# Optimization experiments

Hardware: AMD Instinct MI355X
Metric: run time of the kernel (lower is better)

The kernel has to match this reference:

```python
import jax, jax.numpy as jnp
import numpy as np

N = 20000   # nodes
E = 320000  # edges (before self-loops)
F_IN = 128  # in_feats
H = 4       # heads
C = 64      # hidden (per-head channels; concat=False averages heads)
G = 64      # graphs in batch
EPS = 1e-5  # BatchNorm eps


def _gat(x, src, dst, W, a_src, a_dst, bias):
    # PyG GATConv, concat=False: project, per-edge LeakyReLU attention,
    # segment-softmax over destination nodes, scatter-add, mean over heads.
    h = (x @ W).reshape(N, H, C)                    # [N,H,C]
    es = (h * a_src).sum(-1)                        # [N,H]
    ed = (h * a_dst).sum(-1)                        # [N,H]
    e = jax.nn.leaky_relu(es[src] + ed[dst], 0.2)   # [Etot,H]
    m = jax.ops.segment_max(e, dst, num_segments=N)
    m = jnp.where(jnp.isfinite(m), m, 0.0)          # nodes with no in-edges
    p = jnp.exp(e - m[dst])
    s = jax.ops.segment_sum(p, dst, num_segments=N)
    alpha = p / (s[dst] + 1e-16)                    # PyG softmax epsilon
    out = jax.ops.segment_sum(h[src] * alpha[:, :, None], dst, num_segments=N)
    return out.mean(axis=1) + bias                  # [N,C]


def _bn(x, g, b):
    # BatchNorm1d in training mode: biased batch statistics over nodes
    mu = x.mean(axis=0)
    var = ((x - mu) ** 2).mean(axis=0)
    return (x - mu) * jax.lax.rsqrt(var + EPS) * g + b


def setup_inputs() -> dict:
    key = jax.random.key(0)
    ks = jax.random.split(key, 16)
    x = jax.random.normal(ks[0], (N, F_IN), dtype=jnp.float32)
    edge_index = jax.random.randint(ks[1], (2, E), 0, N, dtype=jnp.int32)
    batch_idx = jnp.sort(jax.random.randint(ks[2], (N,), 0, G, dtype=jnp.int32))
    s1 = 1.0 / np.sqrt(F_IN)
    s2 = 1.0 / np.sqrt(C)
    return {
        "x": x,
        "W1": jax.random.normal(ks[3], (F_IN, H * C), jnp.float32) * s1,
        "a_src1": jax.random.normal(ks[4], (H, C), jnp.float32) * s2,
        "a_dst1": jax.random.normal(ks[5], (H, C), jnp.float32) * s2,
        "b1": jnp.zeros((C,), jnp.float32),
        "Wskip": jax.random.normal(ks[6], (F_IN, C), jnp.float32) * s1,
        "bskip": jnp.zeros((C,), jnp.float32),
        "g1": jnp.ones((C,), jnp.float32),
        "be1": jnp.zeros((C,), jnp.float32),
        "W2": jax.random.normal(ks[7], (C, H * C), jnp.float32) * s2,
        "a_src2": jax.random.normal(ks[8], (H, C), jnp.float32) * s2,
        "a_dst2": jax.random.normal(ks[9], (H, C), jnp.float32) * s2,
        "b2": jnp.zeros((C,), jnp.float32),
        "g2": jnp.ones((C,), jnp.float32),
        "be2": jnp.zeros((C,), jnp.float32),
        "edge_index": edge_index,
        "batch_idx": batch_idx,
    }


def reference(x, W1, a_src1, a_dst1, b1, Wskip, bskip, g1, be1,
              W2, a_src2, a_dst2, b2, g2, be2, edge_index, batch_idx):
    # add self-loops (PyG GATConv default add_self_loops=True)
    loop = jnp.arange(N, dtype=edge_index.dtype)
    src = jnp.concatenate([edge_index[0], loop])
    dst = jnp.concatenate([edge_index[1], loop])

    x0 = x
    h = _gat(x, src, dst, W1, a_src1, a_dst1, b1)
    h = jax.nn.gelu(_bn(h, g1, be1) + x0 @ Wskip + bskip, approximate=False)
    # dropout is identity in eval mode
    h2 = _gat(h, src, dst, W2, a_src2, a_dst2, b2)
    h2 = jax.nn.gelu(_bn(h2, g2, be2) + h, approximate=False)

    # global mean pool over graphs
    sums = jax.ops.segment_sum(h2, batch_idx, num_segments=G)
    cnts = jax.ops.segment_sum(jnp.ones((N,), h2.dtype), batch_idx, num_segments=G)
    return sums / jnp.maximum(cnts, 1.0)[:, None]
```

## Files before the change

### kernel.cpp

```cpp
#include <hip/hip_runtime.h>
#include <math.h>

#define NN   20000
#define EE   320000
#define ETOT 340000
#define FIN  128
#define HH   4
#define CC   64
#define HC   256
#define GG   64
#define BN_EPS 1e-5f
#define S1   384
#define S2   320
#define NBUCK 64
#define MAXDEG 64

typedef _Float16 v8h __attribute__((ext_vector_type(8)));
typedef _Float16 v4h __attribute__((ext_vector_type(4)));
typedef float    v4f __attribute__((ext_vector_type(4)));

__device__ __forceinline__ unsigned short f2bf(float f) {
    unsigned u = __float_as_uint(f);
    unsigned r = (u + 0x7FFF + ((u >> 16) & 1)) >> 16;
    return (unsigned short)r;
}
__device__ __forceinline__ float bf2f(unsigned short u) {
    return __uint_as_float((unsigned)u << 16);
}
__device__ __forceinline__ float gelu_exact(float v) {
    return 0.5f * v * (1.f + erff(v * 0.70710678118654752f));
}

__global__ __launch_bounds__(256) void pre1_kernel(
        const int* __restrict__ bidx, int* __restrict__ gstart,
        const float* __restrict__ W1, const float* __restrict__ Wskip,
        const float* __restrict__ W2,
        const float* __restrict__ as1, const float* __restrict__ ad1,
        const float* __restrict__ as2, const float* __restrict__ ad2,
        _Float16* __restrict__ BT1, _Float16* __restrict__ BT2,
        int* __restrict__ deg, float* __restrict__ sbuck1,
        float* __restrict__ sbuck2, float* __restrict__ outz) {
    int b = blockIdx.x, t = threadIdx.x;
    if (b < 79) {
        int i = b * 256 + t;
        if (i >= NN) return;
        int cur = bidx[i];
        if (i == 0) { for (int g = 0; g <= cur; ++g) gstart[g] = 0; }
        else { int prev = bidx[i - 1]; for (int g = prev + 1; g <= cur; ++g) gstart[g] = i; }
        if (i == NN - 1) { for (int g = cur + 1; g <= GG; ++g) gstart[g] = NN; }
    } else if (b < 271) {
        int i = (b - 79) * 256 + t;
        int col = i >> 7, k = i & 127;
        float v;
        if (col < 256) {
            v = W1[k * 256 + col];
        } else if (col < 320) {
            v = Wskip[k * 64 + (col - 256)];
        } else if (col < 328) {
            int kk = col - 320, h = kk & 3;
            const float* av = (kk < 4 ? as1 : ad1) + h * 64;
            const float* wr = W1 + k * 256 + h * 64;
            float s = 0.f;
            #pragma unroll 8
            for (int c = 0; c < 64; ++c) s += wr[c] * av[c];
            v = s;
        } else v = 0.f;
        BT1[i] = (_Float16)v;
    } else if (b < 351) {
        int i = (b - 271) * 256 + t;
        int col = i >> 6, k = i & 63;
        float v;
        if (col < 256) {
            v = W2[k * 256 + col];
        } else if (col < 264) {
            int kk = col - 256, h = kk & 3;
            const float* av = (kk < 4 ? as2 : ad2) + h * 64;
            const float* wr = W2 + k * 256 + h * 64;
            float s = 0.f;
            #pragma unroll 8
            for (int c = 0; c < 64; ++c) s += wr[c] * av[c];
            v = s;
        } else v = 0.f;
        BT2[i] = (_Float16)v;
    } else if (b < 367) {
        int i = (b - 351) * 256 + t;
        outz[i] = 0.f;
    } else if (b < 446) {
        int i = (b - 367) * 256 + t;
        if (i < NN) deg[i] = 0;
    } else if (b < 478) {
        int i = (b - 446) * 256 + t;
        sbuck1[i] = 0.f;
    } else {
        int i = (b - 478) * 256 + t;
        sbuck2[i] = 0.f;
    }
}

template<int NCB>
__global__ __launch_bounds__(256) void gemm_mfma(const float* __restrict__ A,
        const _Float16* __restrict__ BT, int M, int K,
        unsigned short* __restrict__ h4b, float* __restrict__ skipO,
        float* __restrict__ esf, float* __restrict__ edf,
        int escol0, int ngemm, int do_fill,
        const int* __restrict__ ei, int* __restrict__ deg,
        int* __restrict__ csr) {
    int b = blockIdx.x;
    int t = threadIdx.x;
    if (do_fill && b >= ngemm) {
        int i = (b - ngemm) * 256 + t;
        if (i >= ETOT) return;
        int s, d;
        if (i < EE) { s = ei[i]; d = ei[EE + i]; } else { s = i - EE; d = i - EE; }
        int p = atomicAdd(&deg[d], 1);
        if (p < MAXDEG) csr[d * MAXDEG + p] = s;
        return;
    }
    const int COLT = 2 * NCB * 16;
    __shared__ _Float16 sA[32][40];
    __shared__ _Float16 sBT[2 * NCB * 16][40];
    int row0 = b * 32;
    int wave = t >> 6, lane = t & 63;
    int l15 = lane & 15, quad = lane >> 4;
    int rb  = wave & 1;
    int cb0 = (wave >> 1) * NCB;
    v4f acc[NCB] = {};
    for (int k0 = 0; k0 < K; k0 += 32) {
        {
            int r = t >> 3, c4 = t & 7;
            int gr = row0 + r;
            float4 v0 = make_float4(0.f, 0.f, 0.f, 0.f);
            if (gr < M) v0 = *(const float4*)&A[(size_t)gr * K + k0 + c4 * 4];
            v4h hv;
            hv[0] = (_Float16)v0.x; hv[1] = (_Float16)v0.y;
            hv[2] = (_Float16)v0.z; hv[3] = (_Float16)v0.w;
            *(v4h*)&sA[r][c4 * 4] = hv;
        }
        for (int j = t; j < COLT * 4; j += 256) {
            int c = j >> 2, s = j & 3;
            *(v8h*)&sBT[c][s * 8] = *(const v8h*)&BT[(size_t)c * K + k0 + s * 8];
        }
        __syncthreads();
        v8h af = *(const v8h*)&sA[rb * 16 + l15][quad * 8];
        #pragma unroll
        for (int c = 0; c < NCB; ++c) {
            v8h bf = *(const v8h*)&sBT[(cb0 + c) * 16 + l15][quad * 8];
            acc[c] = __builtin_amdgcn_mfma_f32_16x16x32_f16(af, bf, acc[c], 0, 0, 0);
        }
        __syncthreads();
    }
    #pragma unroll
    for (int c = 0; c < NCB; ++c) {
        int gcol = (cb0 + c) * 16 + l15;
        #pragma unroll
        for (int reg = 0; reg < 4; ++reg) {
            int gr = row0 + rb * 16 + quad * 4 + reg;
            if (gr >= M) continue;
            float v = acc[c][reg];
            if (gcol < 256) {
                h4b[(size_t)gr * HC + gcol] = f2bf(v);
            } else if (skipO != nullptr && gcol < 320) {
                skipO[(size_t)gr * CC + (gcol - 256)] = v;
            } else if (gcol >= escol0 && gcol < escol0 + 8) {
                if (gcol < escol0 + 4) esf[gr * 4 + (gcol - escol0)] = v;
                else                   edf[gr * 4 + (gcol - escol0 - 4)] = v;
            }
        }
    }
}

template<int NCB>
__global__ __launch_bounds__(256) void gemm_mfma_bn(const float* __restrict__ gout,
        const float* __restrict__ skip, const float* __restrict__ sbuck,
        const float* __restrict__ g, const float* __restrict__ be,
        const float* __restrict__ bskip, float* __restrict__ hmid,
        const _Float16* __restrict__ BT, int M, int K,
        unsigned short* __restrict__ h4b,
        float* __restrict__ esf, float* __restrict__ edf, int escol0) {
    const int COLT = 2 * NCB * 16;
    __shared__ _Float16 sA[32][40];
    __shared__ _Float16 sBT[2 * NCB * 16][40];
    __shared__ float tmp[128];
    __shared__ float sscale[64], sshift[64];
    int t = threadIdx.x;
    int b = blockIdx.x;
    if (t < 128) {
        float s = 0.f;
        #pragma unroll 16
        for (int k = 0; k < NBUCK; ++k) s += sbuck[k * 128 + t];
        tmp[t] = s;
    }
    __syncthreads();
    if (t < 64) {
        float mu  = tmp[t] * (1.f / NN);
        float var = tmp[64 + t] * (1.f / NN) - mu * mu;
        float inv = rsqrtf(var + BN_EPS) * g[t];
        sscale[t] = inv;
        sshift[t] = be[t] + bskip[t] - mu * inv;
    }
    __syncthreads();
    int row0 = b * 32;
    int wave = t >> 6, lane = t & 63;
    int l15 = lane & 15, quad = lane >> 4;
    int rb  = wave & 1;
    int cb0 = (wave >> 1) * NCB;
    v4f acc[NCB] = {};
    for (int k0 = 0; k0 < K; k0 += 32) {
        {
            int r = t >> 3, c4 = t & 7;
            int gr = row0 + r;
            int cb = k0 + c4 * 4;
            float vv[4];
            if (gr < M) {
                float4 q = *(const float4*)&gout[(size_t)gr * CC + cb];
                float4 p = *(const float4*)&skip[(size_t)gr * CC + cb];
                float qa[4] = {q.x, q.y, q.z, q.w};
                float pa[4] = {p.x, p.y, p.z, p.w};
                #pragma unroll
                for (int u = 0; u < 4; ++u)
                    vv[u] = gelu_exact(qa[u] * sscale[cb + u] + sshift[cb + u] + pa[u]);
                *(float4*)&hmid[(size_t)gr * CC + cb] =
                    make_float4(vv[0], vv[1], vv[2], vv[3]);
            } else {
                vv[0] = vv[1] = vv[2] = vv[3] = 0.f;
            }
            v4h hv;
            hv[0] = (_Float16)vv[0]; hv[1] = (_Float16)vv[1];
            hv[2] = (_Float16)vv[2]; hv[3] = (_Float16)vv[3];
            *(v4h*)&sA[r][c4 * 4] = hv;
        }
        for (int j = t; j < COLT * 4; j += 256) {
            int c = j >> 2, s = j & 3;
            *(v8h*)&sBT[c][s * 8] = *(const v8h*)&BT[(size_t)c * K + k0 + s * 8];
        }
        __syncthreads();
        v8h af = *(const v8h*)&sA[rb * 16 + l15][quad * 8];
        #pragma unroll
        for (int c = 0; c < NCB; ++c) {
            v8h bf = *(const v8h*)&sBT[(cb0 + c) * 16 + l15][quad * 8];
            acc[c] = __builtin_amdgcn_mfma_f32_16x16x32_f16(af, bf, acc[c], 0, 0, 0);
        }
        __syncthreads();
    }
    #pragma unroll
    for (int c = 0; c < NCB; ++c) {
        int gcol = (cb0 + c) * 16 + l15;
        #pragma unroll
        for (int reg = 0; reg < 4; ++reg) {
            int gr = row0 + rb * 16 + quad * 4 + reg;
            if (gr >= M) continue;
            float v = acc[c][reg];
            if (gcol < 256) {
                h4b[(size_t)gr * HC + gcol] = f2bf(v);
            } else if (gcol >= escol0 && gcol < escol0 + 8) {
                if (gcol < escol0 + 4) esf[gr * 4 + (gcol - escol0)] = v;
                else                   edf[gr * 4 + (gcol - escol0 - 4)] = v;
            }
        }
    }
}

__global__ __launch_bounds__(256) void aggr_kernel(const unsigned short* __restrict__ h4b,
        const float* __restrict__ esf, const float* __restrict__ edf,
        const int* __restrict__ deg, const int* __restrict__ csr_src,
        const float* __restrict__ bias, float* __restrict__ out,
        float* __restrict__ sbuck) {
    int wave = threadIdx.x >> 6, lane = threadIdx.x & 63;
    int head = lane >> 4;
    int n = blockIdx.x * 4 + wave;
    float edn = edf[n * 4 + head];
    float4 acc = make_float4(0.f, 0.f, 0.f, 0.f);
    float ssum = 0.f;
    int dn = deg[n];
    dn = (dn < MAXDEG) ? dn : MAXDEG;
    int beg = n * MAXDEG, end = beg + dn;
    int j = beg;
    for (; j + 4 <= end; j += 4) {
        int4 s4 = *(const int4*)&csr_src[j];
        float E0 = esf[s4.x * 4 + head];
        float E1 = esf[s4.y * 4 + head];
        float E2 = esf[s4.z * 4 + head];
        float E3 = esf[s4.w * 4 + head];
        ushort4 v0 = *(const ushort4*)&h4b[(size_t)s4.x * HC + lane * 4];
        ushort4 v1 = *(const ushort4*)&h4b[(size_t)s4.y * HC + lane * 4];
        ushort4 v2 = *(const ushort4*)&h4b[(size_t)s4.z * HC + lane * 4];
        ushort4 v3 = *(const ushort4*)&h4b[(size_t)s4.w * HC + lane * 4];
        float e0 = E0 + edn; e0 = fmaxf(e0, 0.2f * e0); float w0 = __expf(e0);
        float e1 = E1 + edn; e1 = fmaxf(e1, 0.2f * e1); float w1 = __expf(e1);
        float e2 = E2 + edn; e2 = fmaxf(e2, 0.2f * e2); float w2 = __expf(e2);
        float e3 = E3 + edn; e3 = fmaxf(e3, 0.2f * e3); float w3 = __expf(e3);
        acc.x += w0 * bf2f(v0.x); acc.y += w0 * bf2f(v0.y);
        acc.z += w0 * bf2f(v0.z); acc.w += w0 * bf2f(v0.w); ssum += w0;
        acc.x += w1 * bf2f(v1.x); acc.y += w1 * bf2f(v1.y);
        acc.z += w1 * bf2f(v1.z); acc.w += w1 * bf2f(v1.w); ssum += w1;
        acc.x += w2 * bf2f(v2.x); acc.y += w2 * bf2f(v2.y);
        acc.z += w2 * bf2f(v2.z); acc.w += w2 * bf2f(v2.w); ssum += w2;
        acc.x += w3 * bf2f(v3.x); acc.y += w3 * bf2f(v3.y);
        acc.z += w3 * bf2f(v3.z); acc.w += w3 * bf2f(v3.w); ssum += w3;
    }
    for (; j < end; ++j) {
        int s = csr_src[j];
        float E = esf[s * 4 + head];
        ushort4 v = *(const ushort4*)&h4b[(size_t)s * HC + lane * 4];
        float e = E + edn; e = fmaxf(e, 0.2f * e); float w = __expf(e);
        acc.x += w * bf2f(v.x); acc.y += w * bf2f(v.y);
        acc.z += w * bf2f(v.z); acc.w += w * bf2f(v.w); ssum += w;
    }
    float inv = 1.f / (ssum + 1e-16f);
    float4 r;
    r.x = acc.x * inv; r.y = acc.y * inv; r.z = acc.z * inv; r.w = acc.w * inv;
    r.x += __shfl_xor(r.x, 16); r.y += __shfl_xor(r.y, 16);
    r.z += __shfl_xor(r.z, 16); r.w += __shfl_xor(r.w, 16);
    r.x += __shfl_xor(r.x, 32); r.y += __shfl_xor(r.y, 32);
    r.z += __shfl_xor(r.z, 32); r.w += __shfl_xor(r.w, 32);
    __shared__ float ls[4][64], lq[4][64];
    if (lane < 16) {
        float4 b4 = *(const float4*)&bias[lane * 4];
        float4 o;
        o.x = 0.25f * r.x + b4.x; o.y = 0.25f * r.y + b4.y;
        o.z = 0.25f * r.z + b4.z; o.w = 0.25f * r.w + b4.w;
        *(float4*)&out[n * CC + lane * 4] = o;
        *(float4*)&ls[wave][lane * 4] = o;
        float4 q;
        q.x = o.x * o.x; q.y = o.y * o.y; q.z = o.z * o.z; q.w = o.w * o.w;
        *(float4*)&lq[wave][lane * 4] = q;
    }
    __syncthreads();
    if (wave == 0) {
        float s = ls[0][lane] + ls[1][lane] + ls[2][lane] + ls[3][lane];
        float q = lq[0][lane] + lq[1][lane] + lq[2][lane] + lq[3][lane];
        int bk = (blockIdx.x & (NBUCK - 1)) * 128;
        atomicAdd(&sbuck[bk + lane], s);
        atomicAdd(&sbuck[bk + 64 + lane], q);
    }
}

__global__ __launch_bounds__(256) void bnapply2_kernel(const float* __restrict__ gout,
        const float* __restrict__ sbuck, const float* __restrict__ g,
        const float* __restrict__ be, const float* __restrict__ resid,
        const int* __restrict__ bidx, const int* __restrict__ gstart,
        float* __restrict__ out) {
    __shared__ float tmp[128];
    __shared__ float smu[64], sinv[64];
    __shared__ float ls[4][64];
    __shared__ int gi[4];
    int t = threadIdx.x;
    if (t < 128) {
        float s = 0.f;
        #pragma unroll 16
        for (int k = 0; k < NBUCK; ++k) s += sbuck[k * 128 + t];
        tmp[t] = s;
    }
    __syncthreads();
    if (t < 64) {
        float mu  = tmp[t] * (1.f / NN);
        float var = tmp[64 + t] * (1.f / NN) - mu * mu;
        smu[t] = mu;
        sinv[t] = rsqrtf(var + BN_EPS) * g[t];
    }
    __syncthreads();
    int i = blockIdx.x * 256 + t;
    int ch = i & 63;
    int wave = t >> 6;
    int n = i >> 6;
    float v = (gout[i] - smu[ch]) * sinv[ch] + be[ch] + resid[i];
    v = gelu_exact(v);
    int gg = bidx[n];
    int cnt = gstart[gg + 1] - gstart[gg];
    ls[wave][ch] = v * (1.f / (float)cnt);
    if (ch == 0) gi[wave] = gg;
    __syncthreads();
    if (wave == 0) {
        if (gi[0] == gi[1] && gi[1] == gi[2] && gi[2] == gi[3]) {
            float s = ls[0][ch] + ls[1][ch] + ls[2][ch] + ls[3][ch];
            atomicAdd(&out[gi[0] * CC + ch], s);
        } else {
            #pragma unroll
            for (int w2 = 0; w2 < 4; ++w2)
                atomicAdd(&out[gi[w2] * CC + ch], ls[w2][ch]);
        }
    }
}

extern "C" void kernel_launch(void* const* d_in, const int* in_sizes, int n_in,
                              void* d_out, int out_size, void* d_ws, size_t ws_size,
                              hipStream_t stream) {
    const float* x      = (const float*)d_in[0];
    const float* W1     = (const float*)d_in[1];
    const float* a_src1 = (const float*)d_in[2];
    const float* a_dst1 = (const float*)d_in[3];
    const float* b1     = (const float*)d_in[4];
    const float* Wskip  = (const float*)d_in[5];
    const float* bskip  = (const float*)d_in[6];
    const float* g1     = (const float*)d_in[7];
    const float* be1    = (const float*)d_in[8];
    const float* W2     = (const float*)d_in[9];
    const float* a_src2 = (const float*)d_in[10];
    const float* a_dst2 = (const float*)d_in[11];
    const float* b2     = (const float*)d_in[12];
    const float* g2     = (const float*)d_in[13];
    const float* be2    = (const float*)d_in[14];
    const int*   ei     = (const int*)d_in[15];
    const int*   bidx   = (const int*)d_in[16];
    float* out = (float*)d_out;

    char* w = (char*)d_ws;
    size_t o = 0;
    auto alloc = [&](size_t bytes) -> void* {
        void* p = w + o;
        o = (o + bytes + 255) & ~(size_t)255;
        return p;
    };

    unsigned short* h4b = (unsigned short*)alloc((size_t)NN * HC * 2);
    float* esf = (float*)alloc((size_t)NN * 16);
    float* edf = (float*)alloc((size_t)NN * 16);
    float* skip = (float*)alloc((size_t)NN * CC * 4);
    float* gout = (float*)alloc((size_t)NN * CC * 4);
    float* hmid = (float*)alloc((size_t)NN * CC * 4);
    _Float16* BT1 = (_Float16*)alloc((size_t)S1 * FIN * 2);
    _Float16* BT2 = (_Float16*)alloc((size_t)S2 * CC * 2);
    int* csr    = (int*)alloc((size_t)NN * MAXDEG * 4);
    int* gstart = (int*)alloc((size_t)(GG + 1) * 4);
    int* deg      = (int*)alloc((size_t)NN * 4);
    float* sbuck1 = (float*)alloc((size_t)NBUCK * 128 * 4);
    float* sbuck2 = (float*)alloc((size_t)NBUCK * 128 * 4);

    int ebk = (ETOT + 255) / 256;
    int ngemm = (NN + 31) / 32;
    int nodeblk = NN / 4;

    pre1_kernel<<<510, 256, 0, stream>>>(bidx, gstart,
            W1, Wskip, W2, a_src1, a_dst1, a_src2, a_dst2, BT1, BT2,
            deg, sbuck1, sbuck2, out);

    gemm_mfma<12><<<ngemm + ebk, 256, 0, stream>>>(x, BT1, NN, FIN,
            h4b, skip, esf, edf, 320, ngemm, 1, ei, deg, csr);
    aggr_kernel<<<nodeblk, 256, 0, stream>>>(h4b, esf, edf, deg, csr, b1, gout,
            sbuck1);

    gemm_mfma_bn<10><<<ngemm, 256, 0, stream>>>(gout, skip, sbuck1, g1, be1, bskip,
            hmid, BT2, NN, CC, h4b, esf, edf, 256);
    aggr_kernel<<<nodeblk, 256, 0, stream>>>(h4b, esf, edf, deg, csr, b2, gout,
            sbuck2);
    bnapply2_kernel<<<NN * CC / 256, 256, 0, stream>>>(
        gout, sbuck2, g2, be2, hmid, bidx, gstart, out);
}
```

Measured before the change: 202.6 us.

## Load full K slab once and keep B fragments in registers for MFMA GEMMs

The two projection GEMMs are restructured. Instead of looping over K in 32-wide chunks with a shared-memory B tile and two barriers per step, each block stages the whole 32-row A slab into LDS once. Each wave loads its B fragments straight from global memory into registers and computes both 16-row halves, so every B fragment is reused across two row tiles. The row bounds checks are dropped because N divides evenly by 32, and fewer barriers and LDS round trips are intended. In exchange, register pressure rises and the kernels become specialised to fixed sizes.

After: 212.5 us. 4.9% more time.

```diff
diff --git a/kernel.cpp b/kernel.cpp
--- a/kernel.cpp
+++ b/kernel.cpp
@@ -97,17 +97,15 @@
     }
 }
 
-template<int NCB>
-__global__ __launch_bounds__(256) void gemm_mfma(const float* __restrict__ A,
-        const _Float16* __restrict__ BT, int M, int K,
+__global__ __launch_bounds__(256) void gemm1_kernel(const float* __restrict__ A,
+        const _Float16* __restrict__ BT,
         unsigned short* __restrict__ h4b, float* __restrict__ skipO,
         float* __restrict__ esf, float* __restrict__ edf,
-        int escol0, int ngemm, int do_fill,
-        const int* __restrict__ ei, int* __restrict__ deg,
+        int ngemm, const int* __restrict__ ei, int* __restrict__ deg,
         int* __restrict__ csr) {
     int b = blockIdx.x;
     int t = threadIdx.x;
-    if (do_fill && b >= ngemm) {
+    if (b >= ngemm) {
         int i = (b - ngemm) * 256 + t;
         if (i >= ETOT) return;
         int s, d;
@@ -116,70 +114,78 @@
         if (p < MAXDEG) csr[d * MAXDEG + p] = s;
         return;
     }
-    const int COLT = 2 * NCB * 16;
-    __shared__ _Float16 sA[32][40];
-    __shared__ _Float16 sBT[2 * NCB * 16][40];
+    __shared__ _Float16 sA[32][136];
     int row0 = b * 32;
+    {
+        int r = t >> 3, k0 = (t & 7) * 16;
+        const float* src = &A[(size_t)(row0 + r) * FIN + k0];
+        float4 f0 = *(const float4*)&src[0];
+        float4 f1 = *(const float4*)&src[4];
+        float4 f2 = *(const float4*)&src[8];
+        float4 f3 = *(const float4*)&src[12];
+        v8h h0, h1;
+        h0[0] = (_Float16)f0.x; h0[1] = (_Float16)f0.y;
+        h0[2] = (_Float16)f0.z; h0[3] = (_Float16)f0.w;
+        h0[4] = (_Float16)f1.x; h0[5] = (_Float16)f1.y;
+        h0[6] = (_Float16)f1.z; h0[7] = (_Float16)f1.w;
+        h1[0] = (_Float16)f2.x; h1[1] = (_Float16)f2.y;
+        h1[2] = (_Float16)f2.z; h1[3] = (_Float16)f2.w;
+        h1[4] = (_Float16)f3.x; h1[5] = (_Float16)f3.y;
+        h1[6] = (_Float16)f3.z; h1[7] = (_Float16)f3.w;
+        *(v8h*)&sA[r][k0]     = h0;
+        *(v8h*)&sA[r][k0 + 8] = h1;
+    }
     int wave = t >> 6, lane = t & 63;
     int l15 = lane & 15, quad = lane >> 4;
-    int rb  = wave & 1;
-    int cb0 = (wave >> 1) * NCB;
-    v4f acc[NCB] = {};
-    for (int k0 = 0; k0 < K; k0 += 32) {
-        {
-            int r = t >> 3, c4 = t & 7;
-            int gr = row0 + r;
-            float4 v0 = make_float4(0.f, 0.f, 0.f, 0.f);
-            if (gr < M) v0 = *(const float4*)&A[(size_t)gr * K + k0 + c4 * 4];
-            v4h hv;
-            hv[0] = (_Float16)v0.x; hv[1] = (_Float16)v0.y;
-            hv[2] = (_Float16)v0.z; hv[3] = (_Float16)v0.w;
-            *(v4h*)&sA[r][c4 * 4] = hv;
+    int cb0 = wave * 6;
+    v8h bf[6][4];
+    #pragma unroll
+    for (int c = 0; c < 6; ++c)
+        #pragma unroll
+        for (int k = 0; k < 4; ++k)
+            bf[c][k] = *(const v8h*)&BT[(size_t)((cb0 + c) * 16 + l15) * FIN + k * 32 + quad * 8];
+    __syncthreads();
+    v4f acc[2][6] = {};
+    #pragma unroll
+    for (int k = 0; k < 4; ++k) {
+        v8h a0 = *(const v8h*)&sA[l15][k * 32 + quad * 8];
+        v8h a1 = *(const v8h*)&sA[16 + l15][k * 32 + quad * 8];
+        #pragma unroll
+        for (int c = 0; c < 6; ++c) {
+            acc[0][c] = __builtin_amdgcn_mfma_f32_16x16x32_f16(a0, bf[c][k], acc[0][c], 0, 0, 0);
+            acc[1][c] = __builtin_amdgcn_mfma_f32_16x16x32_f16(a1, bf[c][k], acc[1][c], 0, 0, 0);
         }
-        for (int j = t; j < COLT * 4; j += 256) {
-            int c = j >> 2, s = j & 3;
-            *(v8h*)&sBT[c][s * 8] = *(const v8h*)&BT[(size_t)c * K + k0 + s * 8];
-        }
-        __syncthreads();
-        v8h af = *(const v8h*)&sA[rb * 16 + l15][quad * 8];
-        #pragma unroll
-        for (int c = 0; c < NCB; ++c) {
-            v8h bf = *(const v8h*)&sBT[(cb0 + c) * 16 + l15][quad * 8];
-            acc[c] = __builtin_amdgcn_mfma_f32_16x16x32_f16(af, bf, acc[c], 0, 0, 0);
-        }
-        __syncthreads();
-    }
-    #pragma unroll
-    for (int c = 0; c < NCB; ++c) {
-        int gcol = (cb0 + c) * 16 + l15;
-        #pragma unroll
-        for (int reg = 0; reg < 4; ++reg) {
-            int gr = row0 + rb * 16 + quad * 4 + reg;
-            if (gr >= M) continue;
-            float v = acc[c][reg];
-            if (gcol < 256) {
-                h4b[(size_t)gr * HC + gcol] = f2bf(v);
-            } else if (skipO != nullptr && gcol < 320) {
-                skipO[(size_t)gr * CC + (gcol - 256)] = v;
-            } else if (gcol >= escol0 && gcol < escol0 + 8) {
-                if (gcol < escol0 + 4) esf[gr * 4 + (gcol - escol0)] = v;
-                else                   edf[gr * 4 + (gcol - escol0 - 4)] = v;
+    }
+    #pragma unroll
+    for (int rb = 0; rb < 2; ++rb) {
+        #pragma unroll
+        for (int c = 0; c < 6; ++c) {
+            int gcol = (cb0 + c) * 16 + l15;
+            #pragma unroll
+            for (int reg = 0; reg < 4; ++reg) {
+                int gr = row0 + rb * 16 + quad * 4 + reg;
+                float v = acc[rb][c][reg];
+                if (gcol < 256) {
+                    h4b[(size_t)gr * HC + gcol] = f2bf(v);
+                } else if (gcol < 320) {
+                    skipO[(size_t)gr * CC + (gcol - 256)] = v;
+                } else if (gcol < 328) {
+                    if (gcol < 324) esf[gr * 4 + (gcol - 320)] = v;
+                    else            edf[gr * 4 + (gcol - 324)] = v;
+                }
             }
         }
     }
 }
 
-template<int NCB>
-__global__ __launch_bounds__(256) void gemm_mfma_bn(const float* __restrict__ gout,
+__global__ __launch_bounds__(256) void gemm2_kernel(const float* __restrict__ gout,
         const float* __restrict__ skip, const float* __restrict__ sbuck,
         const float* __restrict__ g, const float* __restrict__ be,
         const float* __restrict__ bskip, float* __restrict__ hmid,
-        const _Float16* __restrict__ BT, int M, int K,
+        const _Float16* __restrict__ BT,
         unsigned short* __restrict__ h4b,
-        float* __restrict__ esf, float* __restrict__ edf, int escol0) {
-    const int COLT = 2 * NCB * 16;
-    __shared__ _Float16 sA[32][40];
-    __shared__ _Float16 sBT[2 * NCB * 16][40];
+        float* __restrict__ esf, float* __restrict__ edf) {
+    __shared__ _Float16 sA[32][72];
     __shared__ float tmp[128];
     __shared__ float sscale[64], sshift[64];
     int t = threadIdx.x;
@@ -200,61 +206,62 @@
     }
     __syncthreads();
     int row0 = b * 32;
+    {
+        int r = t >> 3, c0 = (t & 7) * 8;
+        int gr = row0 + r;
+        float4 q0 = *(const float4*)&gout[(size_t)gr * CC + c0];
+        float4 q1 = *(const float4*)&gout[(size_t)gr * CC + c0 + 4];
+        float4 p0 = *(const float4*)&skip[(size_t)gr * CC + c0];
+        float4 p1 = *(const float4*)&skip[(size_t)gr * CC + c0 + 4];
+        float qa[8] = {q0.x, q0.y, q0.z, q0.w, q1.x, q1.y, q1.z, q1.w};
+        float pa[8] = {p0.x, p0.y, p0.z, p0.w, p1.x, p1.y, p1.z, p1.w};
+        float vv[8];
+        #pragma unroll
+        for (int u = 0; u < 8; ++u)
+            vv[u] = gelu_exact(qa[u] * sscale[c0 + u] + sshift[c0 + u] + pa[u]);
+        *(float4*)&hmid[(size_t)gr * CC + c0]     = make_float4(vv[0], vv[1], vv[2], vv[3]);
+        *(float4*)&hmid[(size_t)gr * CC + c0 + 4] = make_float4(vv[4], vv[5], vv[6], vv[7]);
+        v8h hv;
+        #pragma unroll
+        for (int u = 0; u < 8; ++u) hv[u] = (_Float16)vv[u];
+        *(v8h*)&sA[r][c0] = hv;
+    }
     int wave = t >> 6, lane = t & 63;
     int l15 = lane & 15, quad = lane >> 4;
-    int rb  = wave & 1;
-    int cb0 = (wave >> 1) * NCB;
-    v4f acc[NCB] = {};
-    for (int k0 = 0; k0 < K; k0 += 32) {
-        {
-            int r = t >> 3, c4 = t & 7;
-            int gr = row0 + r;
-            int cb = k0 + c4 * 4;
-            float vv[4];
-            if (gr < M) {
-                float4 q = *(const float4*)&gout[(size_t)gr * CC + cb];
-                float4 p = *(const float4*)&skip[(size_t)gr * CC + cb];
-                float qa[4] = {q.x, q.y, q.z, q.w};
-                float pa[4] = {p.x, p.y, p.z, p.w};
-                #pragma unroll
-                for (int u = 0; u < 4; ++u)
-                    vv[u] = gelu_exact(qa[u] * sscale[cb + u] + sshift[cb + u] + pa[u]);
-                *(float4*)&hmid[(size_t)gr * CC + cb] =
-                    make_float4(vv[0], vv[1], vv[2], vv[3]);
-            } else {
-                vv[0] = vv[1] = vv[2] = vv[3] = 0.f;
-            }
-            v4h hv;
-            hv[0] = (_Float16)vv[0]; hv[1] = (_Float16)vv[1];
-            hv[2] = (_Float16)vv[2]; hv[3] = (_Float16)vv[3];
-            *(v4h*)&sA[r][c4 * 4] = hv;
+    int cb0 = wave * 5;
+    v8h bf[5][2];
+    #pragma unroll
+    for (int c = 0; c < 5; ++c)
+        #pragma unroll
+        for (int k = 0; k < 2; ++k)
+            bf[c][k] = *(const v8h*)&BT[(size_t)((cb0 + c) * 16 + l15) * CC + k * 32 + quad * 8];
+    __syncthreads();
+    v4f acc[2][5] = {};
+    #pragma unroll
+    for (int k = 0; k < 2; ++k) {
+        v8h a0 = *(const v8h*)&sA[l15][k * 32 + quad * 8];
+        v8h a1 = *(const v8h*)&sA[16 + l15][k * 32 + quad * 8];
+        #pragma unroll
+        for (int c = 0; c < 5; ++c) {
+            acc[0][c] = __builtin_amdgcn_mfma_f32_16x16x32_f16(a0, bf[c][k], acc[0][c], 0, 0, 0);
+            acc[1][c] = __builtin_amdgcn_mfma_f32_16x16x32_f16(a1, bf[c][k], acc[1][c], 0, 0, 0);
         }
-        for (int j = t; j < COLT * 4; j += 256) {
-            int c = j >> 2, s = j & 3;
-            *(v8h*)&sBT[c][s * 8] = *(const v8h*)&BT[(size_t)c * K + k0 + s * 8];
-        }
-        __syncthreads();
-        v8h af = *(const v8h*)&sA[rb * 16 + l15][quad * 8];
-        #pragma unroll
-        for (int c = 0; c < NCB; ++c) {
-            v8h bf = *(const v8h*)&sBT[(cb0 + c) * 16 + l15][quad * 8];
-            acc[c] = __builtin_amdgcn_mfma_f32_16x16x32_f16(af, bf, acc[c], 0, 0, 0);
-        }
-        __syncthreads();
-    }
-    #pragma unroll
-    for (int c = 0; c < NCB; ++c) {
-        int gcol = (cb0 + c) * 16 + l15;
-        #pragma unroll
-        for (int reg = 0; reg < 4; ++reg) {
-            int gr = row0 + rb * 16 + quad * 4 + reg;
-            if (gr >= M) continue;
-            float v = acc[c][reg];
-            if (gcol < 256) {
-                h4b[(size_t)gr * HC + gcol] = f2bf(v);
-            } else if (gcol >= escol0 && gcol < escol0 + 8) {
-                if (gcol < escol0 + 4) esf[gr * 4 + (gcol - escol0)] = v;
-                else                   edf[gr * 4 + (gcol - escol0 - 4)] = v;
+    }
+    #pragma unroll
+    for (int rb = 0; rb < 2; ++rb) {
+        #pragma unroll
+        for (int c = 0; c < 5; ++c) {
+            int gcol = (cb0 + c) * 16 + l15;
+            #pragma unroll
+            for (int reg = 0; reg < 4; ++reg) {
+                int gr = row0 + rb * 16 + quad * 4 + reg;
+                float v = acc[rb][c][reg];
+                if (gcol < 256) {
+                    h4b[(size_t)gr * HC + gcol] = f2bf(v);
+                } else if (gcol < 264) {
+                    if (gcol < 260) esf[gr * 4 + (gcol - 256)] = v;
+                    else            edf[gr * 4 + (gcol - 260)] = v;
+                }
             }
         }
     }
@@ -427,20 +434,20 @@
     float* sbuck2 = (float*)alloc((size_t)NBUCK * 128 * 4);
 
     int ebk = (ETOT + 255) / 256;
-    int ngemm = (NN + 31) / 32;
+    int ngemm = NN / 32;
     int nodeblk = NN / 4;
 
     pre1_kernel<<<510, 256, 0, stream>>>(bidx, gstart,
             W1, Wskip, W2, a_src1, a_dst1, a_src2, a_dst2, BT1, BT2,
             deg, sbuck1, sbuck2, out);
 
-    gemm_mfma<12><<<ngemm + ebk, 256, 0, stream>>>(x, BT1, NN, FIN,
-            h4b, skip, esf, edf, 320, ngemm, 1, ei, deg, csr);
+    gemm1_kernel<<<ngemm + ebk, 256, 0, stream>>>(x, BT1,
+            h4b, skip, esf, edf, ngemm, ei, deg, csr);
     aggr_kernel<<<nodeblk, 256, 0, stream>>>(h4b, esf, edf, deg, csr, b1, gout,
             sbuck1);
 
-    gemm_mfma_bn<10><<<ngemm, 256, 0, stream>>>(gout, skip, sbuck1, g1, be1, bskip,
-            hmid, BT2, NN, CC, h4b, esf, edf, 256);
+    gemm2_kernel<<<ngemm, 256, 0, stream>>>(gout, skip, sbuck1, g1, be1, bskip,
+            hmid, BT2, h4b, esf, edf);
     aggr_kernel<<<nodeblk, 256, 0, stream>>>(h4b, esf, edf, deg, csr, b2, gout,
             sbuck2);
     bnapply2_kernel<<<NN * CC / 256, 256, 0, stream>>>(
```
